# Performance work log

Measured on AMD Instinct MI355X. Metric: run time of the kernel, lower is better.

Reference implementation:

```python
import jax, jax.numpy as jnp
import numpy as np
import math

B, S, H = 2, 2048, 2048
NH, HD = 16, 128
THETA = 10000.0
NEG = -1e9


def make_rope_tables(seq_len, head_dim, theta):
    inv_freq = 1.0 / (theta ** (np.arange(0, head_dim, 2, dtype=np.float32) / head_dim))
    pos = np.arange(seq_len, dtype=np.float32)
    freqs = np.outer(pos, inv_freq)                    # (S, HD/2)
    emb = np.concatenate([freqs, freqs], axis=-1)      # (S, HD)
    return jnp.asarray(np.cos(emb)), jnp.asarray(np.sin(emb))


def setup_inputs() -> dict:
    key = jax.random.key(0)
    k1, k2, k3 = jax.random.split(key, 3)
    hidden_states = jax.random.normal(k1, (B, S, H), dtype=jnp.float32)
    rope_cos, rope_sin = make_rope_tables(S, HD, THETA)
    # additive causal mask [1,1,S,S]
    causal = jnp.tril(jnp.ones((S, S), dtype=bool))
    attention_mask = jnp.where(causal, 0.0, NEG).astype(jnp.float32)[None, None]
    w_qkv = jax.random.normal(k2, (3 * H, H), dtype=jnp.float32) * (1.0 / math.sqrt(H))
    w_o = jax.random.normal(k3, (H, H), dtype=jnp.float32) * (1.0 / math.sqrt(H))
    return {"hidden_states": hidden_states, "rope_cos": rope_cos, "rope_sin": rope_sin,
            "attention_mask": attention_mask, "w_qkv": w_qkv, "w_o": w_o}


def apply_rope(x, cos, sin):
    # x: (B, NH, S, HD); cos/sin: (S, HD)
    half = x.shape[-1] // 2
    x1, x2 = x[..., :half], x[..., half:]
    x_rot = jnp.concatenate([-x2, x1], axis=-1)
    return x * cos[None, None] + x_rot * sin[None, None]


def reference(hidden_states, rope_cos, rope_sin, attention_mask, w_qkv, w_o):
    b, s, h = hidden_states.shape
    qkv = hidden_states @ w_qkv.T                      # (B, S, 3H)
    qkv = qkv.reshape(b, s, 3, NH, HD).transpose(2, 0, 3, 1, 4)  # (3, B, NH, S, HD)
    q, k, v = qkv[0], qkv[1], qkv[2]
    q = apply_rope(q, rope_cos, rope_sin)
    k = apply_rope(k, rope_cos, rope_sin)
    scale = 1.0 / math.sqrt(HD)
    scores = jnp.einsum('bhqd,bhkd->bhqk', q, k) * scale + attention_mask
    probs = jax.nn.softmax(scores.astype(jnp.float32), axis=-1).astype(q.dtype)
    out = jnp.einsum('bhqk,bhkd->bhqd', probs, v)      # (B, NH, S, HD)
    out = out.transpose(0, 2, 1, 3).reshape(b, s, h)
    return out @ w_o.T
```

## Files before the change

kernel.cpp:

```cpp
#include <hip/hip_runtime.h>
#include <stdint.h>

typedef unsigned int u32;
typedef unsigned short u16;

typedef __bf16 bf16x8 __attribute__((ext_vector_type(8)));
typedef float f32x4 __attribute__((ext_vector_type(4)));

struct alignas(16) V16 { u32 a, b, c, d; };

__device__ __forceinline__ u16 f2bf(float x) {
    u32 u = __float_as_uint(x);
    u += 0x7FFFu + ((u >> 16) & 1u);
    return (u16)(u >> 16);
}
__device__ __forceinline__ float bf2f(u16 h) {
    return __uint_as_float(((u32)h) << 16);
}

__device__ __forceinline__ bf16x8 ld_frag(const u16* p) {
    return __builtin_bit_cast(bf16x8, *(const V16*)p);
}

__device__ __forceinline__ void async_cp16(u16* lds_dst, const u16* g_src) {
    __builtin_amdgcn_global_load_lds(
        (__attribute__((address_space(1))) void*)g_src,
        (__attribute__((address_space(3))) void*)lds_dst, 16, 0, 0);
}

__global__ __launch_bounds__(256) void cast_all_kernel(
    const float* __restrict__ hidden, const float* __restrict__ wqkv,
    const float* __restrict__ wo,
    u16* __restrict__ hA, u16* __restrict__ wqb, u16* __restrict__ wob)
{
    int i = blockIdx.x * 256 + threadIdx.x;
    const float* src; u16* dst; int off;
    if (i < 2097152)      { src = hidden; dst = hA;  off = i; }
    else if (i < 5242880) { src = wqkv;   dst = wqb; off = i - 2097152; }
    else                  { src = wo;     dst = wob; off = i - 5242880; }
    const float* p = src + (size_t)off * 4;
    ushort4 o;
    o.x = f2bf(p[0]); o.y = f2bf(p[1]); o.z = f2bf(p[2]); o.w = f2bf(p[3]);
    *(ushort4*)(dst + (size_t)off * 4) = o;
}

__global__ __launch_bounds__(256) void gemm_bt(
    const u16* __restrict__ A, const u16* __restrict__ Bt,
    int M, int N, int K, int mode,
    float* __restrict__ Cout,
    u16* __restrict__ Qb, u16* __restrict__ Kb, u16* __restrict__ Vtb)
{
    __shared__ u16 smem[17408];
    u16* As = smem;
    u16* Bs = smem + 8192;

    const int t = threadIdx.x;
    const int w = t >> 6, l = t & 63;
    const int lr = l & 15;
    const int lk = (l >> 4) * 8;

    const int flat = blockIdx.y * gridDim.x + blockIdx.x;
    const int xcd = flat & 7, slot = flat >> 3;
    const int cpx = gridDim.x >> 3;
    const int ncol = xcd * cpx + slot % cpx;
    const int mrow = slot / cpx;
    const int m0 = mrow * 128, n0 = ncol * 128;
    const int wm = (w >> 1) * 64, wn = (w & 1) * 64;

    f32x4 acc[4][4];
#pragma unroll
    for (int i = 0; i < 4; ++i)
#pragma unroll
        for (int j = 0; j < 4; ++j) acc[i][j] = f32x4{0.f, 0.f, 0.f, 0.f};

    const u16* Ag = A + (size_t)m0 * K;
    const u16* Bg = Bt + (size_t)n0 * K;
    const int srow = l >> 2;
    const int scol = (l & 3) * 8;

    for (int k0 = 0; k0 < K; k0 += 64) {
#pragma unroll
        for (int g = 0; g < 2; ++g) {
            const int row = w * 32 + g * 16;
#pragma unroll
            for (int c = 0; c < 2; ++c) {
                async_cp16(&As[c * 4096 + row * 32],
                           Ag + (size_t)(row + srow) * K + k0 + c * 32 + scol);
                async_cp16(&Bs[c * 4096 + row * 32],
                           Bg + (size_t)(row + srow) * K + k0 + c * 32 + scol);
            }
        }
        __syncthreads();

#pragma unroll
        for (int c = 0; c < 2; ++c) {
            bf16x8 af[4], bf[4];
#pragma unroll
            for (int i = 0; i < 4; ++i)
                af[i] = ld_frag(&As[c * 4096 + (wm + i * 16 + lr) * 32 + lk]);
#pragma unroll
            for (int j = 0; j < 4; ++j)
                bf[j] = ld_frag(&Bs[c * 4096 + (wn + j * 16 + lr) * 32 + lk]);
#pragma unroll
            for (int i = 0; i < 4; ++i)
#pragma unroll
                for (int j = 0; j < 4; ++j)
                    acc[i][j] = __builtin_amdgcn_mfma_f32_16x16x32_bf16(af[i], bf[j], acc[i][j], 0, 0, 0);
        }
        __syncthreads();
    }

    const int lrow4 = (l >> 4) * 4;
    if (mode == 1) {
#pragma unroll
        for (int i = 0; i < 4; ++i)
#pragma unroll
            for (int j = 0; j < 4; ++j)
#pragma unroll
                for (int r = 0; r < 4; ++r) {
                    int gr = m0 + wm + i * 16 + lrow4 + r;
                    int gc = n0 + wn + j * 16 + lr;
                    Cout[(size_t)gr * N + gc] = acc[i][j][r];
                }
    } else {
        const int which = n0 >> 11;
        const int nh = (n0 & 2047) >> 7;
        const int bb = m0 >> 11;
        const int s0 = m0 & 2047;
        u16* Cs = smem;
        if (which < 2) {
#pragma unroll
            for (int i = 0; i < 4; ++i)
#pragma unroll
                for (int j = 0; j < 4; ++j)
#pragma unroll
                    for (int r = 0; r < 4; ++r)
                        Cs[(wm + i * 16 + lrow4 + r) * 136 + wn + j * 16 + lr] =
                            f2bf(acc[i][j][r]);
        } else {
#pragma unroll
            for (int i = 0; i < 4; ++i)
#pragma unroll
                for (int j = 0; j < 4; ++j)
#pragma unroll
                    for (int r = 0; r < 4; ++r)
                        Cs[(wn + j * 16 + lr) * 136 + wm + i * 16 + lrow4 + r] =
                            f2bf(acc[i][j][r]);
        }
        __syncthreads();
        const int rrow = t >> 4, rcol = (t & 15) * 8;
        if (which < 2) {
            u16* dst = (which == 0 ? Qb : Kb) +
                       ((size_t)(bb * 16 + nh) * 2048 + s0) * 128;
#pragma unroll
            for (int it = 0; it < 8; ++it) {
                int row = it * 16 + rrow;
                *(V16*)&dst[(size_t)row * 128 + rcol] = *(const V16*)&Cs[row * 136 + rcol];
            }
        } else {
            u16* dst = Vtb + (size_t)(bb * 16 + nh) * 128 * 2048 + s0;
#pragma unroll
            for (int it = 0; it < 8; ++it) {
                int d = it * 16 + rrow;
                *(V16*)&dst[(size_t)d * 2048 + rcol] = *(const V16*)&Cs[d * 136 + rcol];
            }
        }
    }
}

__global__ __launch_bounds__(256) void rope_kernel(
    u16* __restrict__ Qb, u16* __restrict__ Kb,
    const float* __restrict__ cosT, const float* __restrict__ sinT, float qscale)
{
    int idx = blockIdx.x * 256 + threadIdx.x;
    int d = (idx & 7) * 8;
    int s = (idx >> 3) & 2047;
    int bh = idx >> 14;
    size_t base = ((size_t)bh * 2048 + s) * 128;
    float c[8], sn[8];
#pragma unroll
    for (int i = 0; i < 8; ++i) {
        c[i]  = cosT[s * 128 + d + i];
        sn[i] = sinT[s * 128 + d + i];
    }
    union U { V16 v; u16 h[8]; };
    U qlo, qhi, klo, khi, a, bq, ak, bk;
    qlo.v = *(const V16*)&Qb[base + d];
    qhi.v = *(const V16*)&Qb[base + d + 64];
    klo.v = *(const V16*)&Kb[base + d];
    khi.v = *(const V16*)&Kb[base + d + 64];
#pragma unroll
    for (int i = 0; i < 8; ++i) {
        float q1 = bf2f(qlo.h[i]), q2 = bf2f(qhi.h[i]);
        a.h[i]  = f2bf((q1 * c[i] - q2 * sn[i]) * qscale);
        bq.h[i] = f2bf((q2 * c[i] + q1 * sn[i]) * qscale);
        float k1 = bf2f(klo.h[i]), k2 = bf2f(khi.h[i]);
        ak.h[i] = f2bf(k1 * c[i] - k2 * sn[i]);
        bk.h[i] = f2bf(k2 * c[i] + k1 * sn[i]);
    }
    *(V16*)&Qb[base + d]      = a.v;
    *(V16*)&Qb[base + d + 64] = bq.v;
    *(V16*)&Kb[base + d]      = ak.v;
    *(V16*)&Kb[base + d + 64] = bk.v;
}

#define PS_LD 72
__global__ __launch_bounds__(256, 2) void flash_attn(
    const u16* __restrict__ Qb, const u16* __restrict__ Kb, const u16* __restrict__ Vtb,
    u16* __restrict__ ctx)
{
    __shared__ u16 Ks[4 * 64 * 32];
    __shared__ u16 Vts[2 * 128 * 32];
    __shared__ u16 Ps[4 * 16 * PS_LD];

    const int t = threadIdx.x, w = t >> 6, l = t & 63;
    const int lr = l & 15, lk = (l >> 4) * 8, lrow4 = (l >> 4) * 4;
    const int bh = blockIdx.x;
    const int pidx = blockIdx.y;
    const int wm = w * 16;

    const u16* Qg = Qb + (size_t)bh * 2048 * 128;
    const u16* Kg = Kb + (size_t)bh * 2048 * 128;
    const u16* Vg = Vtb + (size_t)bh * 128 * 2048;
    u16* Pw = &Ps[w * 16 * PS_LD];

    const int srow = l >> 2;
    const int scol = (l & 3) * 8;
    const int vh = w & 1, vkc = w >> 1;

    const int b = bh >> 4, nh = bh & 15;

#pragma unroll
    for (int half = 0; half < 2; ++half) {
        const int qt = half ? pidx : 31 - pidx;
        const int q0 = qt * 64;

        bf16x8 qfrag[4];
#pragma unroll
        for (int kc = 0; kc < 4; ++kc)
            qfrag[kc] = ld_frag(&Qg[(size_t)(q0 + wm + lr) * 128 + kc * 32 + lk]);

        f32x4 oacc[8];
#pragma unroll
        for (int jo = 0; jo < 8; ++jo) oacc[jo] = f32x4{0.f, 0.f, 0.f, 0.f};
        float l_part[4] = {0.f, 0.f, 0.f, 0.f};

        const int ktiles = qt + 1;
        for (int kt = 0; kt < ktiles; ++kt) {
            const int c0 = kt * 64;
#pragma unroll
            for (int it = 0; it < 4; ++it)
                async_cp16(&Ks[w * 2048 + it * 512],
                           Kg + (size_t)(c0 + it * 16 + srow) * 128 + w * 32 + scol);
#pragma unroll
            for (int it = 0; it < 4; ++it)
                async_cp16(&Vts[vkc * 4096 + (vh * 64 + it * 16) * 32],
                           Vg + (size_t)(vh * 64 + it * 16 + srow) * 2048 + c0 + vkc * 32 + scol);
            __syncthreads();

            f32x4 pacc[4];
#pragma unroll
            for (int j = 0; j < 4; ++j) pacc[j] = f32x4{0.f, 0.f, 0.f, 0.f};
#pragma unroll
            for (int kc = 0; kc < 4; ++kc) {
                bf16x8 bk[4];
#pragma unroll
                for (int j = 0; j < 4; ++j)
                    bk[j] = ld_frag(&Ks[kc * 2048 + (j * 16 + lr) * 32 + lk]);
#pragma unroll
                for (int j = 0; j < 4; ++j)
                    pacc[j] = __builtin_amdgcn_mfma_f32_16x16x32_bf16(qfrag[kc], bk[j], pacc[j], 0, 0, 0);
            }

            if (kt == qt) {
#pragma unroll
                for (int j = 0; j < 4; ++j) {
                    const int cl = j * 16 + lr;
#pragma unroll
                    for (int r = 0; r < 4; ++r) {
                        float pv = (cl > wm + lrow4 + r) ? 0.f : __expf(pacc[j][r]);
                        pacc[j][r] = pv;
                        l_part[r] += pv;
                    }
                }
            } else {
#pragma unroll
                for (int j = 0; j < 4; ++j)
#pragma unroll
                    for (int r = 0; r < 4; ++r) {
                        float pv = __expf(pacc[j][r]);
                        pacc[j][r] = pv;
                        l_part[r] += pv;
                    }
            }

#pragma unroll
            for (int j = 0; j < 4; ++j)
#pragma unroll
                for (int r = 0; r < 4; ++r)
                    Pw[(lrow4 + r) * PS_LD + j * 16 + lr] = f2bf(pacc[j][r]);

#pragma unroll
            for (int kc = 0; kc < 2; ++kc) {
                bf16x8 ap = ld_frag(&Pw[lr * PS_LD + kc * 32 + lk]);
#pragma unroll
                for (int jo = 0; jo < 8; ++jo) {
                    bf16x8 bv = ld_frag(&Vts[kc * 4096 + (jo * 16 + lr) * 32 + lk]);
                    oacc[jo] = __builtin_amdgcn_mfma_f32_16x16x32_bf16(ap, bv, oacc[jo], 0, 0, 0);
                }
            }
            __syncthreads();
        }

        float linv[4];
#pragma unroll
        for (int r = 0; r < 4; ++r) {
            float s = l_part[r];
#pragma unroll
            for (int dd = 8; dd >= 1; dd >>= 1) s += __shfl_xor(s, dd);
            linv[r] = __builtin_amdgcn_rcpf(s);
        }
#pragma unroll
        for (int jo = 0; jo < 8; ++jo)
#pragma unroll
            for (int r = 0; r < 4; ++r) {
                int srow2 = q0 + wm + lrow4 + r;
                int col = nh * 128 + jo * 16 + lr;
                ctx[((size_t)b * 2048 + srow2) * 2048 + col] = f2bf(oacc[jo][r] * linv[r]);
            }
    }
}

extern "C" void kernel_launch(void* const* d_in, const int* in_sizes, int n_in,
                              void* d_out, int out_size, void* d_ws, size_t ws_size,
                              hipStream_t stream)
{
    (void)in_sizes; (void)n_in; (void)out_size; (void)ws_size;
    const float* hidden = (const float*)d_in[0];
    const float* cosT   = (const float*)d_in[1];
    const float* sinT   = (const float*)d_in[2];
    const float* wqkv   = (const float*)d_in[4];
    const float* wo     = (const float*)d_in[5];
    float* out = (float*)d_out;
    char* ws = (char*)d_ws;

    u16* hA   = (u16*)(ws + 0);
    u16* wqb  = (u16*)(ws + 16777216);
    u16* wob  = (u16*)(ws + 41943040);
    u16* Qb   = (u16*)(ws + 50331648);
    u16* Kb   = (u16*)(ws + 67108864);
    u16* Vtb  = (u16*)(ws + 83886080);
    u16* ctx  = (u16*)(ws + 100663296);

    cast_all_kernel<<<dim3(24576), dim3(256), 0, stream>>>(hidden, wqkv, wo,
                                                           hA, wqb, wob);

    gemm_bt<<<dim3(48, 32), dim3(256), 0, stream>>>(hA, wqb, 4096, 6144, 2048, 0,
                                                    nullptr, Qb, Kb, Vtb);
    rope_kernel<<<dim3(2048), dim3(256), 0, stream>>>(Qb, Kb, cosT, sinT,
                                                      0.08838834764831845f);

    flash_attn<<<dim3(32, 16), dim3(256), 0, stream>>>(Qb, Kb, Vtb, ctx);

    gemm_bt<<<dim3(16, 32), dim3(256), 0, stream>>>(ctx, wob, 4096, 2048, 2048, 1,
                                                    out, nullptr, nullptr, nullptr);
}
```

Baseline: 398.6 us.

## Replace 128x128 GEMM with 256x256 tile, double-buffered async pipeline and swizzled LDS

Both projection GEMMs move to a new 512-thread kernel with 256x256 output tiles, 128KB of dynamic LDS, and a double-buffered cp.async pipeline that prefetches the next K-tiles while MFMAs run. The LDS layout uses XOR swizzles to cut bank conflicts, and s_setprio is raised around the MFMA blocks. The aim is higher arithmetic intensity per loaded byte and overlap of global loads with compute. In exchange the grid is much smaller (384 and 128 blocks), which can underfill the GPU's CUs, especially for the output projection. Register pressure also rises.

```diff
diff --git a/kernel.cpp b/kernel.cpp
--- a/kernel.cpp
+++ b/kernel.cpp
@@ -44,126 +44,181 @@
     *(ushort4*)(dst + (size_t)off * 4) = o;
 }
 
-__global__ __launch_bounds__(256) void gemm_bt(
+__device__ __forceinline__ void stage_half(
+    u16* smem, const u16* __restrict__ Ag, const u16* __restrict__ Bg,
+    int K, int isB, int kk, int buf, int th, int w, int rg0, int chl)
+{
+    const u16* G = isB ? Bg : Ag;
+    u16* base = smem + isB * 32768 + buf * 16384 + kk * 8192;
+    const int kcol = th * 64 + kk * 32;
+#pragma unroll
+    for (int i = 0; i < 2; ++i) {
+        const int s = i * 8 + w;
+        const int rg = s * 16 + rg0;
+        async_cp16(base + s * 512, G + (size_t)rg * K + kcol + chl * 8);
+    }
+}
+
+__global__ __launch_bounds__(512, 2) void gemm256(
     const u16* __restrict__ A, const u16* __restrict__ Bt,
     int M, int N, int K, int mode,
     float* __restrict__ Cout,
     u16* __restrict__ Qb, u16* __restrict__ Kb, u16* __restrict__ Vtb)
 {
-    __shared__ u16 smem[17408];
-    u16* As = smem;
-    u16* Bs = smem + 8192;
-
+    extern __shared__ u16 smem[];
     const int t = threadIdx.x;
     const int w = t >> 6, l = t & 63;
-    const int lr = l & 15;
-    const int lk = (l >> 4) * 8;
+    const int lr = l & 15, lk = (l >> 4) * 8;
+    const int wm16 = (w >> 2) * 8;
+    const int wn16 = (w & 3) * 4;
+    const int laneoff = lr * 32 + (lk ^ ((lr & 8) ? 16 : 0));
+    const int rg0 = l >> 2;
+    const int chl = (l & 3) ^ ((l >> 4) & 2);
 
     const int flat = blockIdx.y * gridDim.x + blockIdx.x;
     const int xcd = flat & 7, slot = flat >> 3;
     const int cpx = gridDim.x >> 3;
     const int ncol = xcd * cpx + slot % cpx;
     const int mrow = slot / cpx;
-    const int m0 = mrow * 128, n0 = ncol * 128;
-    const int wm = (w >> 1) * 64, wn = (w & 1) * 64;
-
-    f32x4 acc[4][4];
-#pragma unroll
-    for (int i = 0; i < 4; ++i)
-#pragma unroll
-        for (int j = 0; j < 4; ++j) acc[i][j] = f32x4{0.f, 0.f, 0.f, 0.f};
+    const int m0 = mrow * 256, n0 = ncol * 256;
 
     const u16* Ag = A + (size_t)m0 * K;
     const u16* Bg = Bt + (size_t)n0 * K;
-    const int srow = l >> 2;
-    const int scol = (l & 3) * 8;
-
-    for (int k0 = 0; k0 < K; k0 += 64) {
-#pragma unroll
-        for (int g = 0; g < 2; ++g) {
-            const int row = w * 32 + g * 16;
-#pragma unroll
-            for (int c = 0; c < 2; ++c) {
-                async_cp16(&As[c * 4096 + row * 32],
-                           Ag + (size_t)(row + srow) * K + k0 + c * 32 + scol);
-                async_cp16(&Bs[c * 4096 + row * 32],
-                           Bg + (size_t)(row + srow) * K + k0 + c * 32 + scol);
+
+    f32x4 acc[8][4];
+#pragma unroll
+    for (int i = 0; i < 8; ++i)
+#pragma unroll
+        for (int j = 0; j < 4; ++j) acc[i][j] = f32x4{0.f, 0.f, 0.f, 0.f};
+
+    const int NT = K >> 6;
+
+    stage_half(smem, Ag, Bg, K, 0, 0, 0, 0, w, rg0, chl);
+    stage_half(smem, Ag, Bg, K, 1, 0, 0, 0, w, rg0, chl);
+    stage_half(smem, Ag, Bg, K, 0, 1, 0, 0, w, rg0, chl);
+    stage_half(smem, Ag, Bg, K, 1, 1, 0, 0, w, rg0, chl);
+    stage_half(smem, Ag, Bg, K, 0, 0, 1, 1, w, rg0, chl);
+    stage_half(smem, Ag, Bg, K, 1, 0, 1, 1, w, rg0, chl);
+    asm volatile("s_waitcnt vmcnt(4)" ::: "memory");
+    __builtin_amdgcn_s_barrier();
+
+    for (int tt = 0; tt < NT; tt += 2) {
+#pragma unroll
+        for (int sub = 0; sub < 2; ++sub) {
+            const int tcur = tt + sub;
+            const u16* Abuf = smem + sub * 16384;
+            const u16* Bbuf = smem + 32768 + sub * 16384;
+            bf16x8 bfr[4];
+#pragma unroll
+            for (int p = 0; p < 4; ++p) {
+                const int kk = p >> 1, mh = p & 1;
+                const u16* Ab = Abuf + kk * 8192;
+                const u16* Bb = Bbuf + kk * 8192;
+                if (mh == 0) {
+#pragma unroll
+                    for (int ni = 0; ni < 4; ++ni)
+                        bfr[ni] = ld_frag(Bb + (wn16 + ni) * 512 + laneoff);
+                }
+                bf16x8 af[4];
+#pragma unroll
+                for (int i = 0; i < 4; ++i)
+                    af[i] = ld_frag(Ab + (wm16 + mh * 4 + i) * 512 + laneoff);
+
+                if (p == 0 && tcur + 1 < NT)
+                    stage_half(smem, Ag, Bg, K, 0, 1, sub ^ 1, tcur + 1, w, rg0, chl);
+                if (p == 1 && tcur + 1 < NT)
+                    stage_half(smem, Ag, Bg, K, 1, 1, sub ^ 1, tcur + 1, w, rg0, chl);
+                if (p == 2 && tcur + 2 < NT)
+                    stage_half(smem, Ag, Bg, K, 0, 0, sub, tcur + 2, w, rg0, chl);
+                if (p == 3 && tcur + 2 < NT)
+                    stage_half(smem, Ag, Bg, K, 1, 0, sub, tcur + 2, w, rg0, chl);
+
+                if (p == 3) {
+                    if (tcur < NT - 2) asm volatile("s_waitcnt vmcnt(4)" ::: "memory");
+                    else               asm volatile("s_waitcnt vmcnt(0)" ::: "memory");
+                }
+                __builtin_amdgcn_s_barrier();
+                __builtin_amdgcn_s_setprio(1);
+#pragma unroll
+                for (int i = 0; i < 4; ++i)
+#pragma unroll
+                    for (int ni = 0; ni < 4; ++ni)
+                        acc[mh * 4 + i][ni] = __builtin_amdgcn_mfma_f32_16x16x32_bf16(
+                            af[i], bfr[ni], acc[mh * 4 + i][ni], 0, 0, 0);
+                __builtin_amdgcn_s_setprio(0);
+                __builtin_amdgcn_s_barrier();
             }
         }
-        __syncthreads();
-
-#pragma unroll
-        for (int c = 0; c < 2; ++c) {
-            bf16x8 af[4], bf[4];
-#pragma unroll
-            for (int i = 0; i < 4; ++i)
-                af[i] = ld_frag(&As[c * 4096 + (wm + i * 16 + lr) * 32 + lk]);
-#pragma unroll
-            for (int j = 0; j < 4; ++j)
-                bf[j] = ld_frag(&Bs[c * 4096 + (wn + j * 16 + lr) * 32 + lk]);
-#pragma unroll
-            for (int i = 0; i < 4; ++i)
-#pragma unroll
-                for (int j = 0; j < 4; ++j)
-                    acc[i][j] = __builtin_amdgcn_mfma_f32_16x16x32_bf16(af[i], bf[j], acc[i][j], 0, 0, 0);
+    }
+
+    __syncthreads();
+    const int lrow4 = (l >> 4) * 4;
+    const int wm0 = (w >> 2) * 128, wn0 = (w & 3) * 64;
+
+    if (mode == 1) {
+#pragma unroll
+        for (int mi = 0; mi < 8; ++mi)
+#pragma unroll
+            for (int ni = 0; ni < 4; ++ni)
+#pragma unroll
+                for (int r = 0; r < 4; ++r) {
+                    int gr = m0 + wm0 + mi * 16 + lrow4 + r;
+                    int gc = n0 + wn0 + ni * 16 + lr;
+                    Cout[(size_t)gr * N + gc] = acc[mi][ni][r];
+                }
+        return;
+    }
+
+    const int which = n0 >> 11;
+    const int nh0 = (n0 & 2047) >> 7;
+    const int bb = m0 >> 11;
+    const int s0 = m0 & 2047;
+
+    if (which < 2) {
+#pragma unroll
+        for (int mi = 0; mi < 8; ++mi)
+#pragma unroll
+            for (int ni = 0; ni < 4; ++ni)
+#pragma unroll
+                for (int r = 0; r < 4; ++r)
+                    smem[(wm0 + mi * 16 + lrow4 + r) * 256 + wn0 + ni * 16 + lr] =
+                        f2bf(acc[mi][ni][r]);
+    } else {
+#pragma unroll
+        for (int mi = 0; mi < 8; ++mi)
+#pragma unroll
+            for (int ni = 0; ni < 4; ++ni)
+#pragma unroll
+                for (int r = 0; r < 4; ++r) {
+                    int cr = wn0 + ni * 16 + lr;
+                    int cc = wm0 + mi * 16 + lrow4 + r;
+                    smem[cr * 256 + (cc ^ ((cr & 7) << 3))] = f2bf(acc[mi][ni][r]);
+                }
+    }
+    __syncthreads();
+
+    if (which < 2) {
+        u16* dstb = (which == 0 ? Qb : Kb);
+#pragma unroll
+        for (int ps = 0; ps < 16; ++ps) {
+            int chunk = ps * 512 + t;
+            int row = chunk >> 5;
+            int ce = (chunk & 31) * 8;
+            int head = nh0 + (ce >> 7);
+            int d = ce & 127;
+            *(V16*)&dstb[((size_t)(bb * 16 + head) * 2048 + s0 + row) * 128 + d] =
+                *(const V16*)&smem[row * 256 + ce];
         }
-        __syncthreads();
-    }
-
-    const int lrow4 = (l >> 4) * 4;
-    if (mode == 1) {
-#pragma unroll
-        for (int i = 0; i < 4; ++i)
-#pragma unroll
-            for (int j = 0; j < 4; ++j)
-#pragma unroll
-                for (int r = 0; r < 4; ++r) {
-                    int gr = m0 + wm + i * 16 + lrow4 + r;
-                    int gc = n0 + wn + j * 16 + lr;
-                    Cout[(size_t)gr * N + gc] = acc[i][j][r];
-                }
     } else {
-        const int which = n0 >> 11;
-        const int nh = (n0 & 2047) >> 7;
-        const int bb = m0 >> 11;
-        const int s0 = m0 & 2047;
-        u16* Cs = smem;
-        if (which < 2) {
-#pragma unroll
-            for (int i = 0; i < 4; ++i)
-#pragma unroll
-                for (int j = 0; j < 4; ++j)
-#pragma unroll
-                    for (int r = 0; r < 4; ++r)
-                        Cs[(wm + i * 16 + lrow4 + r) * 136 + wn + j * 16 + lr] =
-                            f2bf(acc[i][j][r]);
-        } else {
-#pragma unroll
-            for (int i = 0; i < 4; ++i)
-#pragma unroll
-                for (int j = 0; j < 4; ++j)
-#pragma unroll
-                    for (int r = 0; r < 4; ++r)
-                        Cs[(wn + j * 16 + lr) * 136 + wm + i * 16 + lrow4 + r] =
-                            f2bf(acc[i][j][r]);
-        }
-        __syncthreads();
-        const int rrow = t >> 4, rcol = (t & 15) * 8;
-        if (which < 2) {
-            u16* dst = (which == 0 ? Qb : Kb) +
-                       ((size_t)(bb * 16 + nh) * 2048 + s0) * 128;
-#pragma unroll
-            for (int it = 0; it < 8; ++it) {
-                int row = it * 16 + rrow;
-                *(V16*)&dst[(size_t)row * 128 + rcol] = *(const V16*)&Cs[row * 136 + rcol];
-            }
-        } else {
-            u16* dst = Vtb + (size_t)(bb * 16 + nh) * 128 * 2048 + s0;
-#pragma unroll
-            for (int it = 0; it < 8; ++it) {
-                int d = it * 16 + rrow;
-                *(V16*)&dst[(size_t)d * 2048 + rcol] = *(const V16*)&Cs[d * 136 + rcol];
-            }
+#pragma unroll
+        for (int ps = 0; ps < 16; ++ps) {
+            int chunk = ps * 512 + t;
+            int drow = chunk >> 5;
+            int se = (chunk & 31) * 8;
+            int head = nh0 + (drow >> 7);
+            int d = drow & 127;
+            *(V16*)&Vtb[((size_t)(bb * 16 + head) * 128 + d) * 2048 + s0 + se] =
+                *(const V16*)&smem[drow * 256 + (se ^ ((drow & 7) << 3))];
         }
     }
 }
@@ -352,16 +407,23 @@
     u16* Vtb  = (u16*)(ws + 83886080);
     u16* ctx  = (u16*)(ws + 100663296);
 
+    static bool attr_done = false;
+    if (!attr_done) {
+        hipFuncSetAttribute((const void*)gemm256,
+                            hipFuncAttributeMaxDynamicSharedMemorySize, 131072);
+        attr_done = true;
+    }
+
     cast_all_kernel<<<dim3(24576), dim3(256), 0, stream>>>(hidden, wqkv, wo,
                                                            hA, wqb, wob);
 
-    gemm_bt<<<dim3(48, 32), dim3(256), 0, stream>>>(hA, wqb, 4096, 6144, 2048, 0,
-                                                    nullptr, Qb, Kb, Vtb);
+    gemm256<<<dim3(24, 16), dim3(512), 131072, stream>>>(hA, wqb, 4096, 6144, 2048, 0,
+                                                         nullptr, Qb, Kb, Vtb);
     rope_kernel<<<dim3(2048), dim3(256), 0, stream>>>(Qb, Kb, cosT, sinT,
                                                       0.08838834764831845f);
 
     flash_attn<<<dim3(32, 16), dim3(256), 0, stream>>>(Qb, Kb, Vtb, ctx);
 
-    gemm_bt<<<dim3(16, 32), dim3(256), 0, stream>>>(ctx, wob, 4096, 2048, 2048, 1,
-                                                    out, nullptr, nullptr, nullptr);
-}
+    gemm256<<<dim3(8, 16), dim3(512), 131072, stream>>>(ctx, wob, 4096, 2048, 2048, 1,
+                                                        out, nullptr, nullptr, nullptr);
+}
```

Result: faster. 383.9 us (-3.7%).
